# Kernel tuning notes

Hardware: AMD Instinct MI355X
Metric: run time of the kernel (lower is better)

The kernel has to match this reference:

```python
import jax, jax.numpy as jnp
import numpy as np

NEG_INF = -1000000.0


def setup_inputs() -> dict:
    key = jax.random.key(0)
    k1, k2, k3, k4 = jax.random.split(key, 4)
    B, H, Sq, Sp = 256, 512, 256, 256
    q_hiddens = jax.random.normal(k1, (B, H, Sq), dtype=jnp.float32)
    p_hiddens = jax.random.normal(k2, (B, H, Sp), dtype=jnp.float32)
    # masks: 1 = masked-out position (gets NEG_INF in the score), 0 = attended
    q_mask = jax.random.randint(k3, (B, Sq), 0, 2, dtype=jnp.int32)
    p_mask = jax.random.randint(k4, (B, Sp), 0, 2, dtype=jnp.int32)
    return {"q_hiddens": q_hiddens, "p_hiddens": p_hiddens,
            "q_mask": q_mask, "p_mask": p_mask}


def reference(q_hiddens, p_hiddens, q_mask, p_mask):
    # similarity_matrix = bmm(q_hiddens^T, p_hiddens): (B, Sq, Sp)
    sim = jnp.einsum('bhq,bhp->bqp', q_hiddens, p_hiddens)
    # mask_matrix = bmm(q_mask.unsqueeze(2), p_mask.unsqueeze(1)) (outer product)
    mask_matrix = (q_mask[:, :, None] * p_mask[:, None, :]).astype(sim.dtype)
    # masked softmax over the p dimension
    att = jax.nn.softmax(sim + mask_matrix * NEG_INF, axis=2)  # (B, Sq, Sp)
    # q_hiddens_tilda = bmm(att, p_hiddens^T): (B, Sq, H)
    q_tilda = jnp.einsum('bqp,bhp->bqh', att, p_hiddens)
    q_t = jnp.transpose(q_hiddens, (0, 2, 1))  # (B, Sq, H)
    # 4-way feature concat: [h, h~, h-h~, h*h~] -> (B, Sq, 4H)
    q_matching_states = jnp.concatenate(
        [q_t, q_tilda, q_t - q_tilda, q_t * q_tilda], axis=2)
    return q_matching_states
```

## Files before the change

kernel.cpp:

```cpp
#include <hip/hip_runtime.h>

typedef _Float16 half8 __attribute__((ext_vector_type(8)));
typedef float    f32x4 __attribute__((ext_vector_type(4)));

#define NB  256
#define NH  512
#define NSQ 256
#define NSP 256

__global__ __launch_bounds__(256, 2)
void rmatch_kernel(const float* __restrict__ Q, const float* __restrict__ P,
                   const int* __restrict__ QM, const int* __restrict__ PM,
                   float* __restrict__ out)
{
    __shared__ union {
        struct { _Float16 A[64][40];  _Float16 Bm[256][40]; } p1;
        struct { _Float16 P2[32][264]; } p2;
    } stg;
    __shared__ _Float16 att[64][264];
    __shared__ float    qtl[64][36];

    const int tid  = threadIdx.x;
    const int b    = blockIdx.x >> 2;
    const int q0   = (blockIdx.x & 3) << 6;
    const int w    = tid >> 6;
    const int lane = tid & 63;
    const int c    = lane & 15;
    const int g    = lane >> 4;

    const float* Qg = Q + (size_t)b * NH * NSQ;
    const float* Pg = P + (size_t)b * NH * NSP;

    f32x4 acc1[16];
#pragma unroll
    for (int nt = 0; nt < 16; ++nt) { f32x4 z = {0.f,0.f,0.f,0.f}; acc1[nt] = z; }

    const int aL = tid & 63;
    const int aB = tid >> 6;

    for (int kc = 0; kc < 16; ++kc) {
        const int h0 = kc * 32;
        {
            half8 hv;
#pragma unroll
            for (int j = 0; j < 8; ++j)
                hv[j] = (_Float16)Qg[(h0 + aB*8 + j) * NSQ + q0 + aL];
            *(half8*)&stg.p1.A[aL][aB*8] = hv;
        }
#pragma unroll
        for (int it = 0; it < 4; ++it) {
            half8 hv;
#pragma unroll
            for (int j = 0; j < 8; ++j)
                hv[j] = (_Float16)Pg[(h0 + it*8 + j) * NSP + tid];
            *(half8*)&stg.p1.Bm[tid][it*8] = hv;
        }
        __syncthreads();
        half8 av = *(const half8*)&stg.p1.A[16*w + c][g*8];
#pragma unroll
        for (int nt = 0; nt < 16; ++nt) {
            half8 bv = *(const half8*)&stg.p1.Bm[nt*16 + c][g*8];
            acc1[nt] = __builtin_amdgcn_mfma_f32_16x16x32_f16(av, bv, acc1[nt], 0, 0, 0);
        }
        __syncthreads();
    }

    {
        const int* qm = QM + b * NSQ + q0;
        const int* pm = PM + b * NSP;
        int pmv[16];
#pragma unroll
        for (int nt = 0; nt < 16; ++nt) pmv[nt] = pm[nt*16 + c];
#pragma unroll
        for (int reg = 0; reg < 4; ++reg) {
            const int row = 16*w + 4*g + reg;
            const int qmv = qm[row];
            float mx = -3.0e38f;
#pragma unroll
            for (int nt = 0; nt < 16; ++nt) {
                float v = acc1[nt][reg];
                if (qmv & pmv[nt]) v += -1000000.0f;
                acc1[nt][reg] = v;
                mx = fmaxf(mx, v);
            }
#pragma unroll
            for (int xm = 1; xm < 16; xm <<= 1)
                mx = fmaxf(mx, __shfl_xor(mx, xm, 64));
            float s = 0.f;
#pragma unroll
            for (int nt = 0; nt < 16; ++nt) {
                float e = __expf(acc1[nt][reg] - mx);
                acc1[nt][reg] = e;
                s += e;
            }
#pragma unroll
            for (int xm = 1; xm < 16; xm <<= 1)
                s += __shfl_xor(s, xm, 64);
            const float inv = 1.0f / s;
#pragma unroll
            for (int nt = 0; nt < 16; ++nt)
                att[row][nt*16 + c] = (_Float16)(acc1[nt][reg] * inv);
        }
    }
    __syncthreads();

    for (int hc = 0; hc < 16; ++hc) {
        const int h1 = hc * 32;
#pragma unroll
        for (int it = 0; it < 4; ++it) {
            const int tk  = tid + 256*it;
            const int row = tk >> 5;
            const int c8  = tk & 31;
            const float* src = &Pg[(h1 + row) * NSP + c8*8];
            f32x4 x0 = *(const f32x4*)src;
            f32x4 x1 = *(const f32x4*)(src + 4);
            half8 hv;
#pragma unroll
            for (int l = 0; l < 4; ++l) { hv[l] = (_Float16)x0[l]; hv[4+l] = (_Float16)x1[l]; }
            *(half8*)&stg.p2.P2[row][c8*8] = hv;
        }
        __syncthreads();

        f32x4 acc2[2];
        { f32x4 z = {0.f,0.f,0.f,0.f}; acc2[0] = z; acc2[1] = z; }
#pragma unroll
        for (int ks = 0; ks < 8; ++ks) {
            half8 av = *(const half8*)&att[16*w + c][ks*32 + g*8];
#pragma unroll
            for (int nt = 0; nt < 2; ++nt) {
                half8 bv = *(const half8*)&stg.p2.P2[nt*16 + c][ks*32 + g*8];
                acc2[nt] = __builtin_amdgcn_mfma_f32_16x16x32_f16(av, bv, acc2[nt], 0, 0, 0);
            }
        }
#pragma unroll
        for (int nt = 0; nt < 2; ++nt)
#pragma unroll
            for (int reg = 0; reg < 4; ++reg)
                qtl[16*w + 4*g + reg][nt*16 + c] = acc2[nt][reg];
        __syncthreads();

        {
            const int qq = tid >> 2, hg = tid & 3;
            float* ob = out + ((size_t)(b * NSQ + q0 + qq)) * 2048 + h1;
#pragma unroll
            for (int j = 0; j < 2; ++j) {
                const int h4 = hg + 4*j;
                f32x4 t4 = *(const f32x4*)&qtl[qq][h4*4];
                f32x4 qt;
#pragma unroll
                for (int l = 0; l < 4; ++l)
                    qt[l] = Qg[(h1 + h4*4 + l) * NSQ + q0 + qq];
                f32x4 df = qt - t4;
                f32x4 pr = qt * t4;
                *(f32x4*)&ob[        h4*4] = qt;
                *(f32x4*)&ob[ 512  + h4*4] = t4;
                *(f32x4*)&ob[1024  + h4*4] = df;
                *(f32x4*)&ob[1536  + h4*4] = pr;
            }
        }
        __syncthreads();
    }
}

extern "C" void kernel_launch(void* const* d_in, const int* in_sizes, int n_in,
                              void* d_out, int out_size, void* d_ws, size_t ws_size,
                              hipStream_t stream)
{
    const float* Q  = (const float*)d_in[0];
    const float* P  = (const float*)d_in[1];
    const int*   QM = (const int*)d_in[2];
    const int*   PM = (const int*)d_in[3];
    float* o = (float*)d_out;
    rmatch_kernel<<<dim3(NB * 4), dim3(256), 0, stream>>>(Q, P, QM, PM, o);
}
```

Before: 812.0 us.

## Pre-pack Q and P into fp16 MFMA fragment layout in a prep kernel

Adds a prep kernel that converts Q and P to fp16 and writes them to workspace already arranged in MFMA fragment order, both for the first GEMM and for the transposed second GEMM. The main kernel then loads its operands straight from global memory into registers, with no LDS staging and no barriers in the GEMM loops. It also writes outputs directly from the accumulators and swizzles the block order. In exchange it adds an extra kernel launch and a full fp16 copy of the inputs (about 200MB written and read back). The output stores become scalar strided writes instead of vectorized f32x4 stores. The old path is kept as a fallback when the workspace is too small.

```diff
diff --git a/kernel.cpp b/kernel.cpp
--- a/kernel.cpp
+++ b/kernel.cpp
@@ -7,6 +7,177 @@
 #define NH  512
 #define NSQ 256
 #define NSP 256
+
+__global__ __launch_bounds__(256)
+void prep_kernel(const float* __restrict__ Q, const float* __restrict__ P,
+                 _Float16* __restrict__ QAf, _Float16* __restrict__ PBf,
+                 _Float16* __restrict__ PB2f)
+{
+    const int tid  = threadIdx.x;
+    const int w    = tid >> 6;
+    const int lane = tid & 63;
+    const int c    = lane & 15;
+    const int g    = lane >> 4;
+    const int id   = blockIdx.x & 4095;
+    const int b    = id >> 4;
+    const int kc   = id & 15;
+    const int job  = blockIdx.x >> 12;
+
+    if (job == 0) {
+        const float* src = Q + (size_t)b * (NH * NSQ);
+        _Float16* dstb = QAf + (size_t)b * 131072;
+#pragma unroll
+        for (int t = 0; t < 4; ++t) {
+            half8 hv;
+#pragma unroll
+            for (int j = 0; j < 8; ++j)
+                hv[j] = (_Float16)src[(kc*32 + g*8 + j) * NSQ + t*64 + w*16 + c];
+            *(half8*)(dstb + ((size_t)((t*16 + kc)*4 + w))*512 + lane*8) = hv;
+        }
+    } else if (job == 1) {
+        const float* src = P + (size_t)b * (NH * NSP);
+        _Float16* dstb = PBf + (size_t)b * 131072;
+#pragma unroll
+        for (int i = 0; i < 4; ++i) {
+            const int nt = w*4 + i;
+            half8 hv;
+#pragma unroll
+            for (int j = 0; j < 8; ++j)
+                hv[j] = (_Float16)src[(kc*32 + g*8 + j) * NSP + nt*16 + c];
+            *(half8*)(dstb + ((size_t)(kc*16 + nt))*512 + lane*8) = hv;
+        }
+    } else {
+        const float* src = P + (size_t)b * (NH * NSP);
+        _Float16* dstb = PB2f + (size_t)b * 131072;
+        const int hc = kc;
+#pragma unroll
+        for (int i = 0; i < 4; ++i) {
+            const int f  = w*4 + i;
+            const int ks = f >> 1;
+            const int nt = f & 1;
+            const float* s2 = src + (hc*32 + nt*16 + c) * NSP + ks*32 + g*8;
+            f32x4 x0 = *(const f32x4*)s2;
+            f32x4 x1 = *(const f32x4*)(s2 + 4);
+            half8 hv;
+#pragma unroll
+            for (int l = 0; l < 4; ++l) { hv[l] = (_Float16)x0[l]; hv[4+l] = (_Float16)x1[l]; }
+            *(half8*)(dstb + ((size_t)((hc*8 + ks)*2 + nt))*512 + lane*8) = hv;
+        }
+    }
+}
+
+__global__ __launch_bounds__(256, 3)
+void rmatch_main(const float* __restrict__ Q,
+                 const _Float16* __restrict__ QAf,
+                 const _Float16* __restrict__ PBf,
+                 const _Float16* __restrict__ PB2f,
+                 const int* __restrict__ QM, const int* __restrict__ PM,
+                 float* __restrict__ out)
+{
+    __shared__ _Float16 att[8][64][40];
+
+    const int tid  = threadIdx.x;
+    const int lb   = (blockIdx.x & 7) * 128 + (blockIdx.x >> 3);
+    const int b    = lb >> 2;
+    const int t    = lb & 3;
+    const int q0   = t << 6;
+    const int w    = tid >> 6;
+    const int lane = tid & 63;
+    const int c    = lane & 15;
+    const int g    = lane >> 4;
+
+    f32x4 acc1[16];
+#pragma unroll
+    for (int nt = 0; nt < 16; ++nt) { f32x4 z = {0.f,0.f,0.f,0.f}; acc1[nt] = z; }
+
+    const _Float16* Ab = QAf + (size_t)b*131072 + (size_t)(t*64 + w)*512 + (size_t)lane*8;
+    const _Float16* Bb = PBf + (size_t)b*131072 + (size_t)lane*8;
+    for (int kc = 0; kc < 16; ++kc) {
+        half8 av = *(const half8*)(Ab + kc*2048);
+        const _Float16* bp = Bb + (size_t)kc*8192;
+#pragma unroll
+        for (int nt = 0; nt < 16; ++nt) {
+            half8 bv = *(const half8*)(bp + nt*512);
+            acc1[nt] = __builtin_amdgcn_mfma_f32_16x16x32_f16(av, bv, acc1[nt], 0, 0, 0);
+        }
+    }
+
+    {
+        const int* qm = QM + b * NSQ + q0;
+        const int* pm = PM + b * NSP;
+        int pmv[16];
+#pragma unroll
+        for (int nt = 0; nt < 16; ++nt) pmv[nt] = pm[nt*16 + c];
+#pragma unroll
+        for (int reg = 0; reg < 4; ++reg) {
+            const int row = 16*w + 4*g + reg;
+            const int qmv = qm[row];
+            float mx = -3.0e38f;
+#pragma unroll
+            for (int nt = 0; nt < 16; ++nt) {
+                float v = acc1[nt][reg];
+                if (qmv & pmv[nt]) v += -1000000.0f;
+                acc1[nt][reg] = v;
+                mx = fmaxf(mx, v);
+            }
+#pragma unroll
+            for (int xm = 1; xm < 16; xm <<= 1)
+                mx = fmaxf(mx, __shfl_xor(mx, xm, 64));
+            float s = 0.f;
+#pragma unroll
+            for (int nt = 0; nt < 16; ++nt) {
+                float e = __expf(acc1[nt][reg] - mx);
+                acc1[nt][reg] = e;
+                s += e;
+            }
+#pragma unroll
+            for (int xm = 1; xm < 16; xm <<= 1)
+                s += __shfl_xor(s, xm, 64);
+            const float inv = 1.0f / s;
+#pragma unroll
+            for (int nt = 0; nt < 16; ++nt)
+                att[nt >> 1][row][(nt & 1)*16 + c] = (_Float16)(acc1[nt][reg] * inv);
+        }
+    }
+
+    const _Float16* B2 = PB2f + (size_t)b*131072 + (size_t)lane*8;
+    const float*    Qg = Q + (size_t)b * (NH * NSQ);
+
+    for (int hc = 0; hc < 16; ++hc) {
+        float qt[2][4];
+#pragma unroll
+        for (int nt = 0; nt < 2; ++nt)
+#pragma unroll
+            for (int reg = 0; reg < 4; ++reg)
+                qt[nt][reg] = Qg[(hc*32 + nt*16 + c) * NSQ + q0 + 16*w + 4*g + reg];
+
+        f32x4 acc2[2];
+        { f32x4 z = {0.f,0.f,0.f,0.f}; acc2[0] = z; acc2[1] = z; }
+#pragma unroll
+        for (int ks = 0; ks < 8; ++ks) {
+            half8 av2 = *(const half8*)&att[ks][16*w + c][g*8];
+#pragma unroll
+            for (int nt = 0; nt < 2; ++nt) {
+                half8 bv = *(const half8*)(B2 + (size_t)(hc*16 + ks*2 + nt)*512);
+                acc2[nt] = __builtin_amdgcn_mfma_f32_16x16x32_f16(av2, bv, acc2[nt], 0, 0, 0);
+            }
+        }
+#pragma unroll
+        for (int nt = 0; nt < 2; ++nt)
+#pragma unroll
+            for (int reg = 0; reg < 4; ++reg) {
+                const int q  = q0 + 16*w + 4*g + reg;
+                const int h  = hc*32 + nt*16 + c;
+                const float qv = qt[nt][reg];
+                const float tv = acc2[nt][reg];
+                float* ob = out + (size_t)(b * NSQ + q) * 2048 + h;
+                ob[0]    = qv;
+                ob[512]  = tv;
+                ob[1024] = qv - tv;
+                ob[1536] = qv * tv;
+            }
+    }
+}
 
 __global__ __launch_bounds__(256, 2)
 void rmatch_kernel(const float* __restrict__ Q, const float* __restrict__ P,
@@ -146,13 +317,13 @@
             for (int j = 0; j < 2; ++j) {
                 const int h4 = hg + 4*j;
                 f32x4 t4 = *(const f32x4*)&qtl[qq][h4*4];
-                f32x4 qt;
+                f32x4 qtv;
 #pragma unroll
                 for (int l = 0; l < 4; ++l)
-                    qt[l] = Qg[(h1 + h4*4 + l) * NSQ + q0 + qq];
-                f32x4 df = qt - t4;
-                f32x4 pr = qt * t4;
-                *(f32x4*)&ob[        h4*4] = qt;
+                    qtv[l] = Qg[(h1 + h4*4 + l) * NSQ + q0 + qq];
+                f32x4 df = qtv - t4;
+                f32x4 pr = qtv * t4;
+                *(f32x4*)&ob[        h4*4] = qtv;
                 *(f32x4*)&ob[ 512  + h4*4] = t4;
                 *(f32x4*)&ob[1024  + h4*4] = df;
                 *(f32x4*)&ob[1536  + h4*4] = pr;
@@ -171,5 +342,15 @@
     const int*   QM = (const int*)d_in[2];
     const int*   PM = (const int*)d_in[3];
     float* o = (float*)d_out;
-    rmatch_kernel<<<dim3(NB * 4), dim3(256), 0, stream>>>(Q, P, QM, PM, o);
+
+    const size_t need = (size_t)3 * 67108864;
+    if (ws_size >= need && d_ws != nullptr) {
+        _Float16* QAf  = (_Float16*)d_ws;
+        _Float16* PBf  = QAf + 33554432;
+        _Float16* PB2f = PBf + 33554432;
+        prep_kernel<<<dim3(3 * 4096), dim3(256), 0, stream>>>(Q, P, QAf, PBf, PB2f);
+        rmatch_main<<<dim3(NB * 4), dim3(256), 0, stream>>>(Q, QAf, PBf, PB2f, QM, PM, o);
+    } else {
+        rmatch_kernel<<<dim3(NB * 4), dim3(256), 0, stream>>>(Q, P, QM, PM, o);
+    }
 }
```

After: 928.2 us. +14.3%, slower.
